# Kernel optimization log

Measured on AMD Instinct MI355X. Metric: run time of the kernel, lower is better.

## Reference

```python
import jax, jax.numpy as jnp
import numpy as np

IN_FEATURES = 512
NUM_CENTERS = 2048
BATCH = 16384


def setup_inputs() -> dict:
    key = jax.random.key(0)
    kx, kc = jax.random.split(key)
    x = jax.random.normal(kx, (BATCH, IN_FEATURES), dtype=jnp.float32)
    centers = jax.random.normal(kc, (NUM_CENTERS, IN_FEATURES), dtype=jnp.float32)
    beta = jnp.ones((NUM_CENTERS,), dtype=jnp.float32)
    return {"x": x, "centers": centers, "beta": beta}


def reference(x, centers, beta):
    x_sq = jnp.sum(x * x, axis=-1, keepdims=True)            # (B, 1)
    c_sq = jnp.sum(centers * centers, axis=-1)                # (M,)
    cross = jnp.einsum('bd,md->bm', x, centers)               # (B, M)
    dist_sq = x_sq + c_sq[None, :] - 2.0 * cross              # (B, M)
    return jnp.exp(-beta[None, :] * dist_sq)
```

## Files before the change

### kernel.cpp

```cpp
#include <hip/hip_runtime.h>
#include <stdint.h>

#define IN_F   512
#define N_CTR  2048
#define BATCH  16384

#define BM 128
#define BN 128
#define BK 64

using bf16x8  = __attribute__((ext_vector_type(8))) short;
using f32x4   = __attribute__((ext_vector_type(4))) float;
using ushort8 = __attribute__((ext_vector_type(8))) unsigned short;

typedef const __attribute__((address_space(1))) void* gptr_t;
typedef __attribute__((address_space(3))) void* lptr_t;

static __device__ __forceinline__ unsigned short f2bf(float f) {
    uint32_t u = __builtin_bit_cast(uint32_t, f);
    uint32_t r = u + 0x7fffu + ((u >> 16) & 1u);
    return (unsigned short)(r >> 16);
}

__global__ void convert_rows(const float* __restrict__ src,
                             unsigned short* __restrict__ dst,
                             float* __restrict__ sq) {
    const int row  = blockIdx.x;
    const int lane = threadIdx.x;
    const float* rp = src + (size_t)row * IN_F + lane * 8;
    float4 a = *reinterpret_cast<const float4*>(rp);
    float4 b = *reinterpret_cast<const float4*>(rp + 4);
    float ss = a.x*a.x + a.y*a.y + a.z*a.z + a.w*a.w
             + b.x*b.x + b.y*b.y + b.z*b.z + b.w*b.w;
    ushort8 o;
    o[0]=f2bf(a.x); o[1]=f2bf(a.y); o[2]=f2bf(a.z); o[3]=f2bf(a.w);
    o[4]=f2bf(b.x); o[5]=f2bf(b.y); o[6]=f2bf(b.z); o[7]=f2bf(b.w);
    *reinterpret_cast<ushort8*>(dst + (size_t)row * IN_F + lane * 8) = o;
    #pragma unroll
    for (int off = 32; off > 0; off >>= 1) ss += __shfl_down(ss, off);
    if (lane == 0) sq[row] = ss;
}

__launch_bounds__(256, 2)
__global__ void rbf_gemm(const unsigned short* __restrict__ xb,
                         const unsigned short* __restrict__ cb,
                         const float* __restrict__ xsq,
                         const float* __restrict__ csq,
                         const float* __restrict__ beta,
                         float* __restrict__ out) {
    __shared__ unsigned short As[BM * BK];
    __shared__ unsigned short Bs[BN * BK];

    const int tid  = threadIdx.x;
    const int wid  = tid >> 6;
    const int lane = tid & 63;
    const int wr   = wid >> 1;
    const int wc   = wid & 1;

    const int ntn = N_CTR / BN;
    const int tm  = blockIdx.x / ntn;
    const int tn  = blockIdx.x % ntn;

    const int srow = (wid * 4) * 8 + (lane >> 3);
    const int scol = (lane & 7) * 8;
    const unsigned short* gA0 = xb + (size_t)(tm * BM + srow) * IN_F + scol;
    const unsigned short* gB0 = cb + (size_t)(tn * BN + srow) * IN_F + scol;

    f32x4 acc[4][4] = {};

    for (int kt = 0; kt < IN_F / BK; ++kt) {
        const int kbase = kt * BK;
        #pragma unroll
        for (int i = 0; i < 4; ++i) {
            const unsigned short* ga = gA0 + (size_t)(i * 8) * IN_F + kbase;
            const unsigned short* gb = gB0 + (size_t)(i * 8) * IN_F + kbase;
            __builtin_amdgcn_global_load_lds((gptr_t)ga, (lptr_t)(As + (wid * 4 + i) * 512), 16, 0, 0);
            __builtin_amdgcn_global_load_lds((gptr_t)gb, (lptr_t)(Bs + (wid * 4 + i) * 512), 16, 0, 0);
        }
        __syncthreads();

        #pragma unroll
        for (int kk = 0; kk < 2; ++kk) {
            bf16x8 af[4], bfr[4];
            const int kreg = kk * 32 + (lane >> 4) * 8;
            #pragma unroll
            for (int mi = 0; mi < 4; ++mi)
                af[mi] = *reinterpret_cast<const bf16x8*>(
                    &As[(wr * 64 + mi * 16 + (lane & 15)) * BK + kreg]);
            #pragma unroll
            for (int ni = 0; ni < 4; ++ni)
                bfr[ni] = *reinterpret_cast<const bf16x8*>(
                    &Bs[(wc * 64 + ni * 16 + (lane & 15)) * BK + kreg]);
            #pragma unroll
            for (int mi = 0; mi < 4; ++mi)
                #pragma unroll
                for (int ni = 0; ni < 4; ++ni)
                    acc[mi][ni] = __builtin_amdgcn_mfma_f32_16x16x32_bf16(
                        af[mi], bfr[ni], acc[mi][ni], 0, 0, 0);
        }
        __syncthreads();
    }

    const int row0 = tm * BM + wr * 64;
    const int col0 = tn * BN + wc * 64;
    #pragma unroll
    for (int ni = 0; ni < 4; ++ni) {
        const int col = col0 + ni * 16 + (lane & 15);
        const float bt = beta[col];
        const float cs = csq[col];
        #pragma unroll
        for (int mi = 0; mi < 4; ++mi) {
            #pragma unroll
            for (int j = 0; j < 4; ++j) {
                const int row = row0 + mi * 16 + (lane >> 4) * 4 + j;
                const float d = xsq[row] + cs - 2.0f * acc[mi][ni][j];
                out[(size_t)row * N_CTR + col] = __expf(-bt * d);
            }
        }
    }
}

__global__ void rbf_naive(const float* __restrict__ x,
                          const float* __restrict__ c,
                          const float* __restrict__ beta,
                          float* __restrict__ out) {
    __shared__ float xs[IN_F];
    const int row = blockIdx.x;
    const int col = blockIdx.y * 128 + threadIdx.x;
    for (int i = threadIdx.x; i < IN_F; i += 128)
        xs[i] = x[(size_t)row * IN_F + i];
    __syncthreads();
    const float* cp = c + (size_t)col * IN_F;
    float d = 0.f;
    #pragma unroll 4
    for (int k = 0; k < IN_F; k += 4) {
        float4 cv = *reinterpret_cast<const float4*>(cp + k);
        float t0 = xs[k + 0] - cv.x;
        float t1 = xs[k + 1] - cv.y;
        float t2 = xs[k + 2] - cv.z;
        float t3 = xs[k + 3] - cv.w;
        d += t0 * t0 + t1 * t1 + t2 * t2 + t3 * t3;
    }
    out[(size_t)row * N_CTR + col] = __expf(-beta[col] * d);
}

extern "C" void kernel_launch(void* const* d_in, const int* in_sizes, int n_in,
                              void* d_out, int out_size, void* d_ws, size_t ws_size,
                              hipStream_t stream) {
    const float* x    = (const float*)d_in[0];
    const float* c    = (const float*)d_in[1];
    const float* beta = (const float*)d_in[2];
    float* out        = (float*)d_out;

    const size_t need = (size_t)BATCH * IN_F * 2 + (size_t)N_CTR * IN_F * 2
                      + (size_t)BATCH * 4 + (size_t)N_CTR * 4;
    if (ws_size >= need) {
        unsigned short* xbuf = (unsigned short*)d_ws;
        unsigned short* cbuf = xbuf + (size_t)BATCH * IN_F;
        float* xsq = (float*)(cbuf + (size_t)N_CTR * IN_F);
        float* csq = xsq + BATCH;
        convert_rows<<<BATCH, 64, 0, stream>>>(x, xbuf, xsq);
        convert_rows<<<N_CTR, 64, 0, stream>>>(c, cbuf, csq);
        rbf_gemm<<<(BATCH / BM) * (N_CTR / BN), 256, 0, stream>>>(
            xbuf, cbuf, xsq, csq, beta, out);
    } else {
        rbf_naive<<<dim3(BATCH, N_CTR / 128), 128, 0, stream>>>(x, c, beta, out);
    }
}
```

Before: 71.06 us.

## Double-buffer LDS tiles in RBF GEMM and merge the two conversion kernels

Measured after the change: 75.37 us. +6.1%, slower.

```diff
diff --git a/kernel.cpp b/kernel.cpp
--- a/kernel.cpp
+++ b/kernel.cpp
@@ -8,6 +8,7 @@
 #define BM 128
 #define BN 128
 #define BK 64
+#define NKT (IN_F / BK)
 
 using bf16x8  = __attribute__((ext_vector_type(8))) short;
 using f32x4   = __attribute__((ext_vector_type(4))) float;
@@ -22,12 +23,24 @@
     return (unsigned short)(r >> 16);
 }
 
-__global__ void convert_rows(const float* __restrict__ src,
-                             unsigned short* __restrict__ dst,
-                             float* __restrict__ sq) {
-    const int row  = blockIdx.x;
-    const int lane = threadIdx.x;
-    const float* rp = src + (size_t)row * IN_F + lane * 8;
+__global__ void convert_all(const float* __restrict__ x,
+                            const float* __restrict__ c,
+                            unsigned short* __restrict__ xb,
+                            unsigned short* __restrict__ cb,
+                            float* __restrict__ xsq,
+                            float* __restrict__ csq) {
+    const int wave = threadIdx.x >> 6;
+    const int lane = threadIdx.x & 63;
+    const int row  = blockIdx.x * 4 + wave;
+
+    const float* src;
+    unsigned short* dst;
+    float* sq;
+    int r;
+    if (row < BATCH) { src = x; dst = xb; sq = xsq; r = row; }
+    else             { src = c; dst = cb; sq = csq; r = row - BATCH; }
+
+    const float* rp = src + (size_t)r * IN_F + lane * 8;
     float4 a = *reinterpret_cast<const float4*>(rp);
     float4 b = *reinterpret_cast<const float4*>(rp + 4);
     float ss = a.x*a.x + a.y*a.y + a.z*a.z + a.w*a.w
@@ -35,10 +48,10 @@
     ushort8 o;
     o[0]=f2bf(a.x); o[1]=f2bf(a.y); o[2]=f2bf(a.z); o[3]=f2bf(a.w);
     o[4]=f2bf(b.x); o[5]=f2bf(b.y); o[6]=f2bf(b.z); o[7]=f2bf(b.w);
-    *reinterpret_cast<ushort8*>(dst + (size_t)row * IN_F + lane * 8) = o;
+    *reinterpret_cast<ushort8*>(dst + (size_t)r * IN_F + lane * 8) = o;
     #pragma unroll
     for (int off = 32; off > 0; off >>= 1) ss += __shfl_down(ss, off);
-    if (lane == 0) sq[row] = ss;
+    if (lane == 0) sq[r] = ss;
 }
 
 __launch_bounds__(256, 2)
@@ -48,8 +61,8 @@
                          const float* __restrict__ csq,
                          const float* __restrict__ beta,
                          float* __restrict__ out) {
-    __shared__ unsigned short As[BM * BK];
-    __shared__ unsigned short Bs[BN * BK];
+    __shared__ unsigned short As[2][BM * BK];
+    __shared__ unsigned short Bs[2][BN * BK];
 
     const int tid  = threadIdx.x;
     const int wid  = tid >> 6;
@@ -68,17 +81,18 @@
 
     f32x4 acc[4][4] = {};
 
-    for (int kt = 0; kt < IN_F / BK; ++kt) {
+    auto stage = [&](int buf, int kt) {
         const int kbase = kt * BK;
         #pragma unroll
         for (int i = 0; i < 4; ++i) {
             const unsigned short* ga = gA0 + (size_t)(i * 8) * IN_F + kbase;
             const unsigned short* gb = gB0 + (size_t)(i * 8) * IN_F + kbase;
-            __builtin_amdgcn_global_load_lds((gptr_t)ga, (lptr_t)(As + (wid * 4 + i) * 512), 16, 0, 0);
-            __builtin_amdgcn_global_load_lds((gptr_t)gb, (lptr_t)(Bs + (wid * 4 + i) * 512), 16, 0, 0);
+            __builtin_amdgcn_global_load_lds((gptr_t)ga, (lptr_t)(&As[buf][(wid * 4 + i) * 512]), 16, 0, 0);
+            __builtin_amdgcn_global_load_lds((gptr_t)gb, (lptr_t)(&Bs[buf][(wid * 4 + i) * 512]), 16, 0, 0);
         }
-        __syncthreads();
+    };
 
+    auto compute = [&](int buf) {
         #pragma unroll
         for (int kk = 0; kk < 2; ++kk) {
             bf16x8 af[4], bfr[4];
@@ -86,11 +100,11 @@
             #pragma unroll
             for (int mi = 0; mi < 4; ++mi)
                 af[mi] = *reinterpret_cast<const bf16x8*>(
-                    &As[(wr * 64 + mi * 16 + (lane & 15)) * BK + kreg]);
+                    &As[buf][(wr * 64 + mi * 16 + (lane & 15)) * BK + kreg]);
             #pragma unroll
             for (int ni = 0; ni < 4; ++ni)
                 bfr[ni] = *reinterpret_cast<const bf16x8*>(
-                    &Bs[(wc * 64 + ni * 16 + (lane & 15)) * BK + kreg]);
+                    &Bs[buf][(wc * 64 + ni * 16 + (lane & 15)) * BK + kreg]);
             #pragma unroll
             for (int mi = 0; mi < 4; ++mi)
                 #pragma unroll
@@ -98,8 +112,20 @@
                     acc[mi][ni] = __builtin_amdgcn_mfma_f32_16x16x32_bf16(
                         af[mi], bfr[ni], acc[mi][ni], 0, 0, 0);
         }
+    };
+
+    stage(0, 0);
+    __syncthreads();
+
+    int cur = 0;
+    #pragma unroll
+    for (int kt = 0; kt < NKT - 1; ++kt) {
+        stage(cur ^ 1, kt + 1);
+        compute(cur);
         __syncthreads();
+        cur ^= 1;
     }
+    compute(cur);
 
     const int row0 = tm * BM + wr * 64;
     const int col0 = tn * BN + wc * 64;
@@ -159,8 +185,7 @@
         unsigned short* cbuf = xbuf + (size_t)BATCH * IN_F;
         float* xsq = (float*)(cbuf + (size_t)N_CTR * IN_F);
         float* csq = xsq + BATCH;
-        convert_rows<<<BATCH, 64, 0, stream>>>(x, xbuf, xsq);
-        convert_rows<<<N_CTR, 64, 0, stream>>>(c, cbuf, csq);
+        convert_all<<<(BATCH + N_CTR) / 4, 256, 0, stream>>>(x, c, xbuf, cbuf, xsq, csq);
         rbf_gemm<<<(BATCH / BM) * (N_CTR / BN), 256, 0, stream>>>(
             xbuf, cbuf, xsq, csq, beta, out);
     } else {
```
